# Optimization experiments

Measured on AMD Instinct MI355X. Metric: run time of the kernel, lower is better.

The kernel has to match this reference:

```python
import jax, jax.numpy as jnp
import numpy as np

B, S, D, H = 4, 2048, 1024, 16
HD = D // H  # head_dim = 64


def setup_inputs() -> dict:
    key = jax.random.key(0)
    ks = jax.random.split(key, 10)
    sc = 0.02
    return {
        "data": jax.random.normal(ks[0], (B, S, D), jnp.float32),
        "context": jax.random.normal(ks[1], (B, S, D), jnp.float32),
        "Wq": jax.random.normal(ks[2], (D, D), jnp.float32) * sc,
        "bq": jnp.zeros((D,), jnp.float32),
        "Wk": jax.random.normal(ks[3], (D, D), jnp.float32) * sc,
        "bk": jnp.zeros((D,), jnp.float32),
        "Wv": jax.random.normal(ks[4], (D, D), jnp.float32) * sc,
        "bv": jnp.zeros((D,), jnp.float32),
        "Wo": jax.random.normal(ks[5], (D, D), jnp.float32) * sc,
        "bo": jnp.zeros((D,), jnp.float32),
    }


def reference(data, context, Wq, bq, Wk, bk, Wv, bv, Wo, bo):
    # Q/K/V projections (nn.Linear: x @ W^T + b; here weights stored as [in, out])
    Q = data @ Wq + bq            # [B,S,D]
    K = context @ Wk + bk
    V = context @ Wv + bv
    # split heads -> [B,H,S,HD]
    Q = Q.reshape(B, S, H, HD).transpose(0, 2, 1, 3)
    K = K.reshape(B, S, H, HD).transpose(0, 2, 1, 3)
    V = V.reshape(B, S, H, HD).transpose(0, 2, 1, 3)
    scale = jnp.sqrt(jnp.asarray(HD, Q.dtype))
    Z = jnp.einsum("bhqd,bhkd->bhqk", Q, K) / scale   # [B,H,S,S]
    # causal mask: row >= col allowed
    row = jnp.arange(S)[:, None]
    col = jnp.arange(S)[None, :]
    Z = jnp.where(row >= col, Z, jnp.asarray(-jnp.inf, Z.dtype))
    Z = jax.nn.softmax(Z, axis=-1)
    out = jnp.einsum("bhqk,bhkd->bhqd", Z, V)         # [B,H,S,HD]
    out = out.transpose(0, 2, 1, 3).reshape(B, S, D)
    return out @ Wo + bo
```

## Files before the change

### kernel.cpp

```cpp
#include <hip/hip_runtime.h>
#include <hip/hip_bf16.h>

#define B_ 4
#define S_ 2048
#define D_ 1024
#define H_ 16
#define HD_ 64
#define M_ (B_*S_)
#define NTOK (M_*D_)

typedef __bf16 bf16;
typedef __bf16 bf16v4 __attribute__((ext_vector_type(4)));
typedef __bf16 bf16v8 __attribute__((ext_vector_type(8)));
typedef float f32x4 __attribute__((ext_vector_type(4)));
typedef float f32x16 __attribute__((ext_vector_type(16)));

#define GLDS(gp, lp) __builtin_amdgcn_global_load_lds( \
    (const __attribute__((address_space(1))) void*)(gp), \
    (__attribute__((address_space(3))) void*)(lp), 16, 0, 0)

__global__ void prep_kernel(const float* __restrict__ data, const float* __restrict__ ctx,
                            bf16* __restrict__ dataB, bf16* __restrict__ ctxB,
                            const float* __restrict__ W0, const float* __restrict__ W1,
                            const float* __restrict__ W2, const float* __restrict__ W3,
                            bf16* __restrict__ T0, bf16* __restrict__ T1,
                            bf16* __restrict__ T2, bf16* __restrict__ T3,
                            float s0) {
    int bid = blockIdx.x;
    if (bid < 8192) {
        int i = (bid * 256 + (int)threadIdx.x) * 8;
        const float* src; bf16* dst;
        if (i < NTOK) { src = data + i; dst = dataB + i; }
        else          { src = ctx + (i - NTOK); dst = ctxB + (i - NTOK); }
        const float4* p = reinterpret_cast<const float4*>(src);
        float4 x = p[0], y = p[1];
        bf16v8 o;
        o[0] = (bf16)x.x; o[1] = (bf16)x.y; o[2] = (bf16)x.z; o[3] = (bf16)x.w;
        o[4] = (bf16)y.x; o[5] = (bf16)y.y; o[6] = (bf16)y.z; o[7] = (bf16)y.w;
        *reinterpret_cast<bf16v8*>(dst) = o;
    } else {
        __shared__ float tile[32][33];
        int local = bid - 8192;
        int which = local >> 10;
        int rem = local & 1023;
        const float* W = which == 0 ? W0 : which == 1 ? W1 : which == 2 ? W2 : W3;
        bf16* Wt       = which == 0 ? T0 : which == 1 ? T1 : which == 2 ? T2 : T3;
        float scale    = which == 0 ? s0 : 1.f;
        int nb = (rem & 31) * 32, kb = (rem >> 5) * 32;
        int t = threadIdx.x;
        int c = t & 31, r0 = t >> 5;
        for (int i = 0; i < 4; ++i) {
            int r = r0 + i * 8;
            tile[r][c] = W[(size_t)(kb + r) * D_ + nb + c];
        }
        __syncthreads();
        for (int i = 0; i < 4; ++i) {
            int r = r0 + i * 8;
            Wt[(size_t)(nb + r) * D_ + kb + c] = (bf16)(tile[c][r] * scale);
        }
    }
}

__global__ __launch_bounds__(512, 2) void gemm_big_kernel(
        const bf16* __restrict__ dataB, const bf16* __restrict__ ctxB, const bf16* __restrict__ Ob,
        const bf16* __restrict__ WqT, const bf16* __restrict__ WkT,
        const bf16* __restrict__ WvT, const bf16* __restrict__ WoT,
        const float* __restrict__ bq, const float* __restrict__ bk,
        const float* __restrict__ bv, const float* __restrict__ bo,
        bf16* __restrict__ Qb, bf16* __restrict__ Kb, bf16* __restrict__ Vt,
        float* __restrict__ outp, float qscale, int zofs) {
    __shared__ bf16 Asm[2][256 * 64];
    __shared__ bf16 Bsm[2][128 * 64];
    int z = blockIdx.z + zofs;
    const bf16* A; const bf16* Bt; const float* bias; float bscale = 1.f;
    if (z == 0)      { A = dataB; Bt = WqT; bias = bq; bscale = qscale; }
    else if (z == 1) { A = ctxB;  Bt = WkT; bias = bk; }
    else if (z == 2) { A = ctxB;  Bt = WvT; bias = bv; }
    else             { A = Ob;    Bt = WoT; bias = bo; }

    int mb = blockIdx.x * 256, nb = blockIdx.y * 128;
    int t = threadIdx.x, l = t & 63, w = t >> 6;
    int wr = w >> 1, wc = w & 1;
    int lg = l >> 4, lr = l & 15;
    f32x4 acc[4][4] = {};
    int srow = t >> 3, schk = t & 7;

    auto stage = [&](int k0, int buf) {
        #pragma unroll
        for (int p = 0; p < 4; ++p) {
            int row = p * 64 + srow;
            int cs = schk ^ (row & 7);
            GLDS(&A[(size_t)(mb + row) * D_ + k0 + cs * 8], &Asm[buf][(size_t)(p * 512 + t) * 8]);
        }
        #pragma unroll
        for (int p = 0; p < 2; ++p) {
            int row = p * 64 + srow;
            int cs = schk ^ (row & 7);
            GLDS(&Bt[(size_t)(nb + row) * D_ + k0 + cs * 8], &Bsm[buf][(size_t)(p * 512 + t) * 8]);
        }
    };

    stage(0, 0);
    __syncthreads();
    for (int tt = 0; tt < 16; ++tt) {
        int cur = tt & 1;
        if (tt < 15) stage((tt + 1) * 64, cur ^ 1);
        #pragma unroll
        for (int kk = 0; kk < 2; ++kk) {
            bf16v8 af[4], bfv[4];
            #pragma unroll
            for (int i = 0; i < 4; ++i) {
                int ra = wr * 64 + i * 16 + lr;
                af[i]  = *(const bf16v8*)&Asm[cur][ra * 64 + (((kk * 4 + lg) ^ (ra & 7)) * 8)];
                int rb = wc * 64 + i * 16 + lr;
                bfv[i] = *(const bf16v8*)&Bsm[cur][rb * 64 + (((kk * 4 + lg) ^ (rb & 7)) * 8)];
            }
            #pragma unroll
            for (int i = 0; i < 4; ++i)
                #pragma unroll
                for (int j = 0; j < 4; ++j)
                    acc[i][j] = __builtin_amdgcn_mfma_f32_16x16x32_bf16(af[i], bfv[j], acc[i][j], 0, 0, 0);
        }
        __syncthreads();
    }

    #pragma unroll
    for (int i = 0; i < 4; ++i)
        #pragma unroll
        for (int j = 0; j < 4; ++j) {
            int col = nb + wc * 64 + j * 16 + lr;
            float bvv = bias[col] * bscale;
            int row0 = mb + wr * 64 + i * 16 + lg * 4;
            if (z == 2) {
                int b = row0 >> 11, s = row0 & 2047;
                int bh = b * 16 + (col >> 6), hd = col & 63;
                bf16v4 ov;
                #pragma unroll
                for (int r = 0; r < 4; ++r) ov[r] = (bf16)(acc[i][j][r] + bvv);
                *(bf16v4*)&Vt[((size_t)bh * 64 + hd) * 2048 + s] = ov;
            } else if (z == 3) {
                #pragma unroll
                for (int r = 0; r < 4; ++r)
                    outp[(size_t)(row0 + r) * D_ + col] = acc[i][j][r] + bvv;
            } else {
                bf16* dst = (z == 0) ? Qb : Kb;
                #pragma unroll
                for (int r = 0; r < 4; ++r)
                    dst[(size_t)(row0 + r) * D_ + col] = (bf16)(acc[i][j][r] + bvv);
            }
        }
}

__global__ __launch_bounds__(256, 2) void attn_kernel(const bf16* __restrict__ Q,
                                                      const bf16* __restrict__ Kb,
                                                      const bf16* __restrict__ Vt,
                                                      bf16* __restrict__ O) {
    __shared__ bf16 Ksm[2][64 * 64];
    __shared__ bf16 Vsm[2][64 * 64];

    int id = (int)blockIdx.x;
    int bh = id & 63;
    int qi = (S_ / 128 - 1) - (id >> 6);
    int qb = qi * 128;
    int b = bh >> 4, h = bh & 15;
    int t = threadIdx.x, w = t >> 6, l = t & 63;
    int ln = l & 31, hi = l >> 5;
    int qwave = qb + w * 32;
    int q = qwave + ln;

    const bf16* kbase = Kb + (size_t)(b * S_) * D_ + h * HD_;
    const bf16* vbase = Vt + (size_t)bh * HD_ * S_;
    const bf16* qptr  = Q + (size_t)(b * S_ + q) * D_ + h * HD_;

    bf16v8 qf[4];
    #pragma unroll
    for (int c = 0; c < 4; ++c)
        qf[c] = *(const bf16v8*)(qptr + c * 16 + hi * 8);

    bf16v8 ones;
    #pragma unroll
    for (int e = 0; e < 8; ++e) ones[e] = (bf16)1.0f;

    f32x16 o0 = {}, o1 = {};
    f32x16 ls = {};

    int srow = t >> 3, schk = t & 7;
    int nT = 2 * qi + 2;

    auto stage = [&](int kv0, int bufsel) {
        #pragma unroll
        for (int p = 0; p < 2; ++p) {
            int row = p * 32 + srow;
            int cs = schk ^ (row & 7);
            GLDS(kbase + (size_t)(kv0 + row) * D_ + cs * 8, &Ksm[bufsel][p * 2048 + t * 8]);
            GLDS(vbase + (size_t)row * S_ + kv0 + cs * 8,   &Vsm[bufsel][p * 2048 + t * 8]);
        }
    };

    stage(0, 0);
    for (int tt = 0; tt < nT; ++tt) {
        int cur = tt & 1;
        int kv0 = tt * 64;
        __syncthreads();
        if (tt + 1 < nT) stage(kv0 + 64, cur ^ 1);
        if (kv0 > qwave + 31) continue;

        f32x16 st0 = {}, st1 = {};
        __builtin_amdgcn_s_setprio(1);
        #pragma unroll
        for (int c = 0; c < 4; ++c) {
            int r0 = ln;
            bf16v8 kf0 = *(const bf16v8*)&Ksm[cur][r0 * 64 + (((2 * c + hi) ^ (r0 & 7)) * 8)];
            st0 = __builtin_amdgcn_mfma_f32_32x32x16_bf16(kf0, qf[c], st0, 0, 0, 0);
            int r1 = 32 + ln;
            bf16v8 kf1 = *(const bf16v8*)&Ksm[cur][r1 * 64 + (((2 * c + hi) ^ (r1 & 7)) * 8)];
            st1 = __builtin_amdgcn_mfma_f32_32x32x16_bf16(kf1, qf[c], st1, 0, 0, 0);
        }
        __builtin_amdgcn_s_setprio(0);

        if (kv0 + 63 > qwave) {
            #pragma unroll
            for (int rg = 0; rg < 16; ++rg) {
                int kvo = (rg & 3) + 8 * (rg >> 2) + 4 * hi;
                if (kv0 + kvo > q)      st0[rg] = -__builtin_inff();
                if (kv0 + 32 + kvo > q) st1[rg] = -__builtin_inff();
            }
        }

        #pragma unroll
        for (int i = 0; i < 16; ++i) {
            st0[i] = __builtin_exp2f(st0[i]);
            st1[i] = __builtin_exp2f(st1[i]);
        }

        uint32_t x0[4][2], x1[4][2];
        #pragma unroll
        for (int j = 0; j < 4; ++j) {
            asm("v_cvt_pk_bf16_f32 %0, %1, %2" : "=v"(x0[j][0]) : "v"(st0[4*j+0]), "v"(st0[4*j+1]));
            asm("v_cvt_pk_bf16_f32 %0, %1, %2" : "=v"(x0[j][1]) : "v"(st0[4*j+2]), "v"(st0[4*j+3]));
            asm("v_cvt_pk_bf16_f32 %0, %1, %2" : "=v"(x1[j][0]) : "v"(st1[4*j+0]), "v"(st1[4*j+1]));
            asm("v_cvt_pk_bf16_f32 %0, %1, %2" : "=v"(x1[j][1]) : "v"(st1[4*j+2]), "v"(st1[4*j+3]));
        }
        union PB { uint32_t u[4]; bf16v8 v; };
        PB pb[4];
        #pragma unroll
        for (int c = 0; c < 4; ++c) {
            uint32_t (*xs)[2] = (c >> 1) ? x1 : x0;
            int cp = c & 1;
            #pragma unroll
            for (int d = 0; d < 2; ++d) {
                uint32_t own_lo = xs[2 * cp][d];
                uint32_t own_hi = xs[2 * cp + 1][d];
                uint32_t par_lo = __shfl_xor(own_lo, 32, 64);
                uint32_t par_hi = __shfl_xor(own_hi, 32, 64);
                pb[c].u[d]     = hi ? par_hi : own_lo;
                pb[c].u[2 + d] = hi ? own_hi : par_lo;
            }
        }

        __builtin_amdgcn_s_setprio(1);
        #pragma unroll
        for (int c = 0; c < 4; ++c) {
            int r0 = ln;
            bf16v8 va0 = *(const bf16v8*)&Vsm[cur][r0 * 64 + (((2 * c + hi) ^ (r0 & 7)) * 8)];
            o0 = __builtin_amdgcn_mfma_f32_32x32x16_bf16(va0, pb[c].v, o0, 0, 0, 0);
            int r1 = 32 + ln;
            bf16v8 va1 = *(const bf16v8*)&Vsm[cur][r1 * 64 + (((2 * c + hi) ^ (r1 & 7)) * 8)];
            o1 = __builtin_amdgcn_mfma_f32_32x32x16_bf16(va1, pb[c].v, o1, 0, 0, 0);
            ls = __builtin_amdgcn_mfma_f32_32x32x16_bf16(ones, pb[c].v, ls, 0, 0, 0);
        }
        __builtin_amdgcn_s_setprio(0);
    }

    float li = 1.f / ls[0];
    bf16* obase = O + (size_t)(b * S_ + q) * D_ + h * HD_;
    #pragma unroll
    for (int j = 0; j < 4; ++j) {
        bf16v4 ov;
        #pragma unroll
        for (int r = 0; r < 4; ++r) ov[r] = (bf16)(o0[4 * j + r] * li);
        *(bf16v4*)(obase + 8 * j + 4 * hi) = ov;
    }
    #pragma unroll
    for (int j = 0; j < 4; ++j) {
        bf16v4 ov;
        #pragma unroll
        for (int r = 0; r < 4; ++r) ov[r] = (bf16)(o1[4 * j + r] * li);
        *(bf16v4*)(obase + 32 + 8 * j + 4 * hi) = ov;
    }
}

extern "C" void kernel_launch(void* const* d_in, const int* in_sizes, int n_in,
                              void* d_out, int out_size, void* d_ws, size_t ws_size,
                              hipStream_t stream) {
    const float* data    = (const float*)d_in[0];
    const float* context = (const float*)d_in[1];
    const float* Wq = (const float*)d_in[2];
    const float* bq = (const float*)d_in[3];
    const float* Wk = (const float*)d_in[4];
    const float* bk = (const float*)d_in[5];
    const float* Wv = (const float*)d_in[6];
    const float* bv = (const float*)d_in[7];
    const float* Wo = (const float*)d_in[8];
    const float* bo = (const float*)d_in[9];
    float* out = (float*)d_out;

    char* ws = (char*)d_ws;
    size_t off = 0;
    auto alloc = [&](size_t bytes) { void* p = ws + off; off += (bytes + 255) & ~255ull; return p; };
    bf16* dataB = (bf16*)alloc((size_t)M_ * D_ * 2);
    bf16* ctxB  = (bf16*)alloc((size_t)M_ * D_ * 2);
    bf16* WqT   = (bf16*)alloc((size_t)D_ * D_ * 2);
    bf16* WkT   = (bf16*)alloc((size_t)D_ * D_ * 2);
    bf16* WvT   = (bf16*)alloc((size_t)D_ * D_ * 2);
    bf16* WoT   = (bf16*)alloc((size_t)D_ * D_ * 2);
    bf16* Qb    = (bf16*)alloc((size_t)M_ * D_ * 2);
    bf16* Kb    = (bf16*)alloc((size_t)M_ * D_ * 2);
    bf16* Vt    = (bf16*)alloc((size_t)M_ * D_ * 2);
    bf16* Ob    = ctxB;

    const float qscale = 0.125f * 1.44269504088896340736f;

    prep_kernel<<<12288, 256, 0, stream>>>(data, context, dataB, ctxB,
                                           Wq, Wk, Wv, Wo, WqT, WkT, WvT, WoT, qscale);

    gemm_big_kernel<<<dim3(M_ / 256, D_ / 128, 3), 512, 0, stream>>>(
        dataB, ctxB, Ob, WqT, WkT, WvT, WoT, bq, bk, bv, bo, Qb, Kb, Vt, out, qscale, 0);

    attn_kernel<<<dim3(S_ / 128 * B_ * H_), 256, 0, stream>>>(Qb, Kb, Vt, Ob);

    gemm_big_kernel<<<dim3(M_ / 256, D_ / 128, 1), 512, 0, stream>>>(
        dataB, ctxB, Ob, WqT, WkT, WvT, WoT, bq, bk, bv, bo, Qb, Kb, Vt, out, qscale, 3);
}
```

Before: 191.7 us.

## Replace double-buffered 256x128 GEMM with single-buffered 128x128 tiles

The projection GEMM moves from a 512-thread 256x128 tile with double-buffered LDS staging to a 256-thread 128x128 tile that uses a single LDS buffer and syncs before and after each load. This cuts LDS use and launches twice as many smaller blocks, which could raise occupancy. In exchange, global-to-LDS loads no longer overlap with MFMA compute, and each block gets less operand reuse.

```diff
diff --git a/kernel.cpp b/kernel.cpp
--- a/kernel.cpp
+++ b/kernel.cpp
@@ -61,7 +61,7 @@
     }
 }
 
-__global__ __launch_bounds__(512, 2) void gemm_big_kernel(
+__global__ __launch_bounds__(256) void gemm_qkvo_kernel(
         const bf16* __restrict__ dataB, const bf16* __restrict__ ctxB, const bf16* __restrict__ Ob,
         const bf16* __restrict__ WqT, const bf16* __restrict__ WkT,
         const bf16* __restrict__ WvT, const bf16* __restrict__ WoT,
@@ -69,8 +69,8 @@
         const float* __restrict__ bv, const float* __restrict__ bo,
         bf16* __restrict__ Qb, bf16* __restrict__ Kb, bf16* __restrict__ Vt,
         float* __restrict__ outp, float qscale, int zofs) {
-    __shared__ bf16 Asm[2][256 * 64];
-    __shared__ bf16 Bsm[2][128 * 64];
+    __shared__ bf16 Asm[128 * 64];
+    __shared__ bf16 Bsm[128 * 64];
     int z = blockIdx.z + zofs;
     const bf16* A; const bf16* Bt; const float* bias; float bscale = 1.f;
     if (z == 0)      { A = dataB; Bt = WqT; bias = bq; bscale = qscale; }
@@ -78,42 +78,32 @@
     else if (z == 2) { A = ctxB;  Bt = WvT; bias = bv; }
     else             { A = Ob;    Bt = WoT; bias = bo; }
 
-    int mb = blockIdx.x * 256, nb = blockIdx.y * 128;
+    int mb = blockIdx.x * 128, nb = blockIdx.y * 128;
     int t = threadIdx.x, l = t & 63, w = t >> 6;
     int wr = w >> 1, wc = w & 1;
     int lg = l >> 4, lr = l & 15;
     f32x4 acc[4][4] = {};
-    int srow = t >> 3, schk = t & 7;
-
-    auto stage = [&](int k0, int buf) {
+    int srow = t >> 3;
+    int schk = t & 7;
+    for (int k0 = 0; k0 < D_; k0 += 64) {
+        __syncthreads();
         #pragma unroll
         for (int p = 0; p < 4; ++p) {
-            int row = p * 64 + srow;
-            int cs = schk ^ (row & 7);
-            GLDS(&A[(size_t)(mb + row) * D_ + k0 + cs * 8], &Asm[buf][(size_t)(p * 512 + t) * 8]);
-        }
-        #pragma unroll
-        for (int p = 0; p < 2; ++p) {
-            int row = p * 64 + srow;
-            int cs = schk ^ (row & 7);
-            GLDS(&Bt[(size_t)(nb + row) * D_ + k0 + cs * 8], &Bsm[buf][(size_t)(p * 512 + t) * 8]);
-        }
-    };
-
-    stage(0, 0);
-    __syncthreads();
-    for (int tt = 0; tt < 16; ++tt) {
-        int cur = tt & 1;
-        if (tt < 15) stage((tt + 1) * 64, cur ^ 1);
+            int row = p * 32 + srow;
+            int ca = schk ^ (row & 7);
+            GLDS(&A[(size_t)(mb + row) * D_ + k0 + ca * 8], &Asm[(size_t)(p * 256 + t) * 8]);
+            GLDS(&Bt[(size_t)(nb + row) * D_ + k0 + ca * 8], &Bsm[(size_t)(p * 256 + t) * 8]);
+        }
+        __syncthreads();
         #pragma unroll
         for (int kk = 0; kk < 2; ++kk) {
             bf16v8 af[4], bfv[4];
             #pragma unroll
             for (int i = 0; i < 4; ++i) {
                 int ra = wr * 64 + i * 16 + lr;
-                af[i]  = *(const bf16v8*)&Asm[cur][ra * 64 + (((kk * 4 + lg) ^ (ra & 7)) * 8)];
+                af[i]  = *(const bf16v8*)&Asm[ra * 64 + (((kk * 4 + lg) ^ (ra & 7)) * 8)];
                 int rb = wc * 64 + i * 16 + lr;
-                bfv[i] = *(const bf16v8*)&Bsm[cur][rb * 64 + (((kk * 4 + lg) ^ (rb & 7)) * 8)];
+                bfv[i] = *(const bf16v8*)&Bsm[rb * 64 + (((kk * 4 + lg) ^ (rb & 7)) * 8)];
             }
             #pragma unroll
             for (int i = 0; i < 4; ++i)
@@ -121,9 +111,7 @@
                 for (int j = 0; j < 4; ++j)
                     acc[i][j] = __builtin_amdgcn_mfma_f32_16x16x32_bf16(af[i], bfv[j], acc[i][j], 0, 0, 0);
         }
-        __syncthreads();
-    }
-
+    }
     #pragma unroll
     for (int i = 0; i < 4; ++i)
         #pragma unroll
@@ -324,11 +312,11 @@
     prep_kernel<<<12288, 256, 0, stream>>>(data, context, dataB, ctxB,
                                            Wq, Wk, Wv, Wo, WqT, WkT, WvT, WoT, qscale);
 
-    gemm_big_kernel<<<dim3(M_ / 256, D_ / 128, 3), 512, 0, stream>>>(
+    gemm_qkvo_kernel<<<dim3(M_ / 128, D_ / 128, 3), 256, 0, stream>>>(
         dataB, ctxB, Ob, WqT, WkT, WvT, WoT, bq, bk, bv, bo, Qb, Kb, Vt, out, qscale, 0);
 
     attn_kernel<<<dim3(S_ / 128 * B_ * H_), 256, 0, stream>>>(Qb, Kb, Vt, Ob);
 
-    gemm_big_kernel<<<dim3(M_ / 256, D_ / 128, 1), 512, 0, stream>>>(
+    gemm_qkvo_kernel<<<dim3(M_ / 128, D_ / 128, 1), 256, 0, stream>>>(
         dataB, ctxB, Ob, WqT, WkT, WvT, WoT, bq, bk, bv, bo, Qb, Kb, Vt, out, qscale, 3);
 }
```

Result: faster. 175.2 us, median of 4 (-8.6%).
